# Kernel optimization log

Hardware: AMD Instinct MI355X
Metric: run time of the kernel (lower is better)

The kernel has to match this reference:

```python
import jax, jax.numpy as jnp
import numpy as np

NEG_MASK_SCALE = -1e-09  # faithful to source (source uses -1e-09, likely intended -1e9)


def setup_inputs() -> dict:
    key0 = jax.random.key(0)
    ks = jax.random.split(key0, 7)
    B, Q, K, H = 4, 256, 1024, 128
    return {
        "query": jax.random.normal(ks[0], (B, Q, H), dtype=jnp.float32),
        "key": jax.random.normal(ks[1], (B, K, H), dtype=jnp.float32),
        "value": jax.random.normal(ks[2], (B, K, H), dtype=jnp.float32),
        "mask": jax.random.randint(ks[3], (B, Q, K), 0, 2).astype(jnp.int32),
        "Wq": jax.random.normal(ks[4], (H, H), dtype=jnp.float32) * (1.0 / np.sqrt(H)),
        "Wk": jax.random.normal(ks[5], (H, H), dtype=jnp.float32) * (1.0 / np.sqrt(H)),
        "v": jax.random.normal(ks[6], (H,), dtype=jnp.float32) * (1.0 / np.sqrt(H)),
    }


def reference(query, key, value, mask, Wq, Wk, v):
    # Projections: torch Linear computes x @ W.T
    q_proj = jnp.einsum("bqd,hd->bqh", query, Wq)  # (B, Q, H)
    k_proj = jnp.einsum("bkd,hd->bkh", key, Wk)    # (B, K, H)
    # Additive (Bahdanau) score: v . tanh(q_proj[:, :, None] + k_proj[:, None])
    feat = jnp.tanh(q_proj[:, :, None, :] + k_proj[:, None, :, :])  # (B, Q, K, H)
    score = jnp.einsum("bqkh,h->bqk", feat, v)                      # (B, Q, K)
    score = score + NEG_MASK_SCALE * (1.0 - mask.astype(score.dtype))
    attention_weights = jax.nn.softmax(score, axis=-1)              # (B, Q, K)
    context_vector = jnp.einsum("bqk,bkv->bqv", attention_weights, value)  # (B, Q, V)
    return attention_weights, context_vector
```

## Files before the change

kernel.cpp:

```cpp
#include <hip/hip_runtime.h>

#define Bb 4
#define Qn 256
#define Kn 1024
#define Hn 128
#define QT 4

constexpr float SCALE = 2.88539008177792681f;

#if __has_builtin(__builtin_amdgcn_exp2f)
#define EXP2F(x) __builtin_amdgcn_exp2f(x)
#else
#define EXP2F(x) exp2f(x)
#endif
#if __has_builtin(__builtin_amdgcn_rcpf)
#define RCPF(x) __builtin_amdgcn_rcpf(x)
#else
#define RCPF(x) (1.0f / (x))
#endif

__global__ __launch_bounds__(128) void proj_kernel(const float* __restrict__ query,
                                                   const float* __restrict__ key,
                                                   const float* __restrict__ Wq,
                                                   const float* __restrict__ Wk,
                                                   float* __restrict__ eq,
                                                   float* __restrict__ ekT) {
    __shared__ float4 xs[128];
    const int tid = threadIdx.x;
    const bool isQ = blockIdx.x < (Bb * Qn / 4);
    const int r0 = (isQ ? blockIdx.x : blockIdx.x - Bb * Qn / 4) * 4;
    const float* x = isQ ? query : key;
    const float* W = isQ ? Wq : Wk;

    xs[tid] = ((const float4*)(x + (size_t)r0 * Hn))[tid];
    __syncthreads();
    const float4* W4 = (const float4*)W + (size_t)tid * (Hn / 4);
    float acc0 = 0.f, acc1 = 0.f, acc2 = 0.f, acc3 = 0.f;
#pragma unroll 8
    for (int d = 0; d < Hn / 4; ++d) {
        float4 w = W4[d];
        float4 a0 = xs[d];
        float4 a1 = xs[32 + d];
        float4 a2 = xs[64 + d];
        float4 a3 = xs[96 + d];
        acc0 = fmaf(w.x, a0.x, fmaf(w.y, a0.y, fmaf(w.z, a0.z, fmaf(w.w, a0.w, acc0))));
        acc1 = fmaf(w.x, a1.x, fmaf(w.y, a1.y, fmaf(w.z, a1.z, fmaf(w.w, a1.w, acc1))));
        acc2 = fmaf(w.x, a2.x, fmaf(w.y, a2.y, fmaf(w.z, a2.z, fmaf(w.w, a2.w, acc2))));
        acc3 = fmaf(w.x, a3.x, fmaf(w.y, a3.y, fmaf(w.z, a3.z, fmaf(w.w, a3.w, acc3))));
    }
    if (isQ) {
        eq[(size_t)(r0 + 0) * Hn + tid] = EXP2F(acc0 * SCALE);
        eq[(size_t)(r0 + 1) * Hn + tid] = EXP2F(acc1 * SCALE);
        eq[(size_t)(r0 + 2) * Hn + tid] = EXP2F(acc2 * SCALE);
        eq[(size_t)(r0 + 3) * Hn + tid] = EXP2F(acc3 * SCALE);
    } else {
        const int b = r0 / Kn;
        const int k0 = r0 % Kn;
        float4 res = make_float4(EXP2F(acc0 * SCALE), EXP2F(acc1 * SCALE),
                                 EXP2F(acc2 * SCALE), EXP2F(acc3 * SCALE));
        ((float4*)ekT)[(size_t)(b * Hn + tid) * (Kn / 4) + (k0 >> 2)] = res;
    }
}

__global__ __launch_bounds__(1024) void fused_attn_kernel(const float* __restrict__ eq,
                                                          const float* __restrict__ ekT,
                                                          const float* __restrict__ v,
                                                          const float* __restrict__ value,
                                                          float* __restrict__ attn,
                                                          float* __restrict__ ctx) {
    const int tid = threadIdx.x;
    const int q0 = blockIdx.x * QT;
    const int b = blockIdx.y;

    __shared__ __align__(16) float4 qs4[Hn];
    __shared__ float vs[Hn];
    __shared__ __align__(16) float sc[QT][Kn];
    __shared__ float red[16][QT];
    __shared__ __align__(16) float4 pl[8][QT][Hn / 4];

    if (tid < Hn) vs[tid] = v[tid];
    if (tid < QT * Hn) {
        const int q = tid >> 7, h = tid & 127;
        ((float*)&qs4[h])[q] = eq[((size_t)b * Qn + q0 + q) * Hn + h];
    }
    __syncthreads();

    const int k = tid;
    const float* ek = ekT + (size_t)b * Hn * Kn + k;
    float a0 = 0.f, a1 = 0.f, a2 = 0.f, a3 = 0.f;
#pragma unroll 8
    for (int h = 0; h < Hn; ++h) {
        const float kv = ek[(size_t)h * Kn];
        const float4 qv = qs4[h];
        const float vh = vs[h];
        float r;
        r = RCPF(fmaf(qv.x, kv, 1.0f)); a0 = fmaf(vh, r, a0);
        r = RCPF(fmaf(qv.y, kv, 1.0f)); a1 = fmaf(vh, r, a1);
        r = RCPF(fmaf(qv.z, kv, 1.0f)); a2 = fmaf(vh, r, a2);
        r = RCPF(fmaf(qv.w, kv, 1.0f)); a3 = fmaf(vh, r, a3);
    }

    const int lane = tid & 63, wv = tid >> 6;
    float m0 = a0, m1 = a1, m2 = a2, m3 = a3;
#pragma unroll
    for (int off = 32; off; off >>= 1) {
        m0 = fminf(m0, __shfl_xor(m0, off));
        m1 = fminf(m1, __shfl_xor(m1, off));
        m2 = fminf(m2, __shfl_xor(m2, off));
        m3 = fminf(m3, __shfl_xor(m3, off));
    }
    if (lane == 0) {
        red[wv][0] = m0; red[wv][1] = m1; red[wv][2] = m2; red[wv][3] = m3;
    }
    __syncthreads();
    m0 = red[0][0]; m1 = red[0][1]; m2 = red[0][2]; m3 = red[0][3];
#pragma unroll
    for (int w = 1; w < 16; ++w) {
        m0 = fminf(m0, red[w][0]); m1 = fminf(m1, red[w][1]);
        m2 = fminf(m2, red[w][2]); m3 = fminf(m3, red[w][3]);
    }
    __syncthreads();

    float e0 = EXP2F((m0 - a0) * SCALE);
    float e1 = EXP2F((m1 - a1) * SCALE);
    float e2 = EXP2F((m2 - a2) * SCALE);
    float e3 = EXP2F((m3 - a3) * SCALE);
    float s0 = e0, s1 = e1, s2 = e2, s3 = e3;
#pragma unroll
    for (int off = 32; off; off >>= 1) {
        s0 += __shfl_xor(s0, off);
        s1 += __shfl_xor(s1, off);
        s2 += __shfl_xor(s2, off);
        s3 += __shfl_xor(s3, off);
    }
    if (lane == 0) {
        red[wv][0] = s0; red[wv][1] = s1; red[wv][2] = s2; red[wv][3] = s3;
    }
    __syncthreads();
    s0 = red[0][0]; s1 = red[0][1]; s2 = red[0][2]; s3 = red[0][3];
#pragma unroll
    for (int w = 1; w < 16; ++w) {
        s0 += red[w][0]; s1 += red[w][1]; s2 += red[w][2]; s3 += red[w][3];
    }

    const float w0 = e0 * RCPF(s0);
    const float w1 = e1 * RCPF(s1);
    const float w2 = e2 * RCPF(s2);
    const float w3 = e3 * RCPF(s3);
    sc[0][k] = w0; sc[1][k] = w1; sc[2][k] = w2; sc[3][k] = w3;
    float* arow = attn + ((size_t)b * Qn + q0) * Kn + k;
    arow[0 * Kn] = w0; arow[1 * Kn] = w1; arow[2 * Kn] = w2; arow[3 * Kn] = w3;
    __syncthreads();

    const int kc = tid >> 7;
    const int cq = (tid >> 5) & 3;
    const int h4 = tid & 31;
    const float4* vb = (const float4*)(value + ((size_t)b * Kn + kc * 128) * Hn) + h4;
    const float* wr = &sc[cq][kc * 128];
    float4 acc = make_float4(0.f, 0.f, 0.f, 0.f);
#pragma unroll 4
    for (int kk = 0; kk < 128; ++kk) {
        const float wgt = wr[kk];
        const float4 vv = vb[(size_t)kk * (Hn / 4)];
        acc.x = fmaf(wgt, vv.x, acc.x);
        acc.y = fmaf(wgt, vv.y, acc.y);
        acc.z = fmaf(wgt, vv.z, acc.z);
        acc.w = fmaf(wgt, vv.w, acc.w);
    }
    pl[kc][cq][h4] = acc;
    __syncthreads();
    if (tid < QT * Hn / 4) {
        const int q = tid >> 5, h = tid & 31;
        float4 r0 = pl[0][q][h], r1 = pl[1][q][h], r2 = pl[2][q][h], r3 = pl[3][q][h];
        float4 r4 = pl[4][q][h], r5 = pl[5][q][h], r6 = pl[6][q][h], r7 = pl[7][q][h];
        float4 sum;
        sum.x = ((r0.x + r1.x) + (r2.x + r3.x)) + ((r4.x + r5.x) + (r6.x + r7.x));
        sum.y = ((r0.y + r1.y) + (r2.y + r3.y)) + ((r4.y + r5.y) + (r6.y + r7.y));
        sum.z = ((r0.z + r1.z) + (r2.z + r3.z)) + ((r4.z + r5.z) + (r6.z + r7.z));
        sum.w = ((r0.w + r1.w) + (r2.w + r3.w)) + ((r4.w + r5.w) + (r6.w + r7.w));
        ((float4*)(ctx + ((size_t)b * Qn + q0 + q) * Hn))[h] = sum;
    }
}

extern "C" void kernel_launch(void* const* d_in, const int* in_sizes, int n_in,
                              void* d_out, int out_size, void* d_ws, size_t ws_size,
                              hipStream_t stream) {
    const float* query = (const float*)d_in[0];
    const float* key = (const float*)d_in[1];
    const float* value = (const float*)d_in[2];
    const float* Wq = (const float*)d_in[4];
    const float* Wk = (const float*)d_in[5];
    const float* v = (const float*)d_in[6];

    float* out = (float*)d_out;
    float* attn = out;
    float* ctx = out + (size_t)Bb * Qn * Kn;

    float* ws = (float*)d_ws;
    float* eq = ws;
    float* ekT = ws + 131072;

    proj_kernel<<<dim3(Bb * Qn / 4 + Bb * Kn / 4), dim3(128), 0, stream>>>(
        query, key, Wq, Wk, eq, ekT);
    fused_attn_kernel<<<dim3(Qn / QT, Bb), dim3(1024), 0, stream>>>(
        eq, ekT, v, value, attn, ctx);
}
```

Before: 117.7 us.

## Double-buffer key and value tiles through LDS with register prefetch

The score loop now stages the transposed exp-key matrix through a two-slot shared-memory buffer, eight h-rows at a time. The next chunk is prefetched into registers while the current chunk is computed from LDS. The weighted-value accumulation is restructured the same way, streaming 64-row value chunks through the same buffer, with each k-group handling 8 rows per chunk. This is meant to hide global-memory latency behind the reciprocal/FMA work. In exchange it adds about 64KB of LDS and a block barrier per chunk, roughly 32 extra syncs per block.

```diff
diff --git a/kernel.cpp b/kernel.cpp
--- a/kernel.cpp
+++ b/kernel.cpp
@@ -5,6 +5,10 @@
 #define Kn 1024
 #define Hn 128
 #define QT 4
+#define CH 8
+#define NCH (Hn / CH)
+#define CKV 64
+#define NCKV (Kn / CKV)
 
 constexpr float SCALE = 2.88539008177792681f;
 
@@ -72,6 +76,7 @@
     const int q0 = blockIdx.x * QT;
     const int b = blockIdx.y;
 
+    __shared__ __align__(16) float stage[2][CH * Kn];
     __shared__ __align__(16) float4 qs4[Hn];
     __shared__ float vs[Hn];
     __shared__ __align__(16) float sc[QT][Kn];
@@ -83,21 +88,45 @@
         const int q = tid >> 7, h = tid & 127;
         ((float*)&qs4[h])[q] = eq[((size_t)b * Qn + q0 + q) * Hn + h];
     }
-    __syncthreads();
-
-    const int k = tid;
-    const float* ek = ekT + (size_t)b * Hn * Kn + k;
+
+    const float* ekb = ekT + (size_t)b * Hn * Kn;
+    {
+        const float4* s = (const float4*)ekb;
+        float4 tA = s[tid], tB = s[tid + 1024];
+        ((float4*)&stage[0][0])[tid] = tA;
+        ((float4*)&stage[0][0])[tid + 1024] = tB;
+    }
+    __syncthreads();
+
     float a0 = 0.f, a1 = 0.f, a2 = 0.f, a3 = 0.f;
-#pragma unroll 8
-    for (int h = 0; h < Hn; ++h) {
-        const float kv = ek[(size_t)h * Kn];
-        const float4 qv = qs4[h];
-        const float vh = vs[h];
-        float r;
-        r = RCPF(fmaf(qv.x, kv, 1.0f)); a0 = fmaf(vh, r, a0);
-        r = RCPF(fmaf(qv.y, kv, 1.0f)); a1 = fmaf(vh, r, a1);
-        r = RCPF(fmaf(qv.z, kv, 1.0f)); a2 = fmaf(vh, r, a2);
-        r = RCPF(fmaf(qv.w, kv, 1.0f)); a3 = fmaf(vh, r, a3);
+    for (int c = 0; c < NCH; ++c) {
+        const int cur = c & 1;
+        const bool more = (c + 1 < NCH);
+        float4 tA, tB;
+        if (more) {
+            const float4* s = (const float4*)(ekb + (size_t)(c + 1) * CH * Kn);
+            tA = s[tid];
+            tB = s[tid + 1024];
+        }
+        const float* sb = &stage[cur][0];
+#pragma unroll
+        for (int j = 0; j < CH; ++j) {
+            const int h = c * CH + j;
+            const float kv = sb[j * Kn + tid];
+            const float4 qv = qs4[h];
+            const float vh = vs[h];
+            float r;
+            r = RCPF(fmaf(qv.x, kv, 1.0f)); a0 = fmaf(vh, r, a0);
+            r = RCPF(fmaf(qv.y, kv, 1.0f)); a1 = fmaf(vh, r, a1);
+            r = RCPF(fmaf(qv.z, kv, 1.0f)); a2 = fmaf(vh, r, a2);
+            r = RCPF(fmaf(qv.w, kv, 1.0f)); a3 = fmaf(vh, r, a3);
+        }
+        if (more) {
+            float* db = &stage[cur ^ 1][0];
+            ((float4*)db)[tid] = tA;
+            ((float4*)db)[tid + 1024] = tB;
+        }
+        __syncthreads();
     }
 
     const int lane = tid & 63, wv = tid >> 6;
@@ -143,6 +172,7 @@
         s0 += red[w][0]; s1 += red[w][1]; s2 += red[w][2]; s3 += red[w][3];
     }
 
+    const int k = tid;
     const float w0 = e0 * RCPF(s0);
     const float w1 = e1 * RCPF(s1);
     const float w2 = e2 * RCPF(s2);
@@ -150,24 +180,49 @@
     sc[0][k] = w0; sc[1][k] = w1; sc[2][k] = w2; sc[3][k] = w3;
     float* arow = attn + ((size_t)b * Qn + q0) * Kn + k;
     arow[0 * Kn] = w0; arow[1 * Kn] = w1; arow[2 * Kn] = w2; arow[3 * Kn] = w3;
-    __syncthreads();
-
-    const int kc = tid >> 7;
+
+    const float* vbase = value + (size_t)b * Kn * Hn;
+    {
+        const float4* s = (const float4*)vbase;
+        float4 tA = s[tid], tB = s[tid + 1024];
+        __syncthreads();
+        ((float4*)&stage[0][0])[tid] = tA;
+        ((float4*)&stage[0][0])[tid + 1024] = tB;
+    }
+    __syncthreads();
+
+    const int kc2 = tid >> 7;
     const int cq = (tid >> 5) & 3;
     const int h4 = tid & 31;
-    const float4* vb = (const float4*)(value + ((size_t)b * Kn + kc * 128) * Hn) + h4;
-    const float* wr = &sc[cq][kc * 128];
     float4 acc = make_float4(0.f, 0.f, 0.f, 0.f);
-#pragma unroll 4
-    for (int kk = 0; kk < 128; ++kk) {
-        const float wgt = wr[kk];
-        const float4 vv = vb[(size_t)kk * (Hn / 4)];
-        acc.x = fmaf(wgt, vv.x, acc.x);
-        acc.y = fmaf(wgt, vv.y, acc.y);
-        acc.z = fmaf(wgt, vv.z, acc.z);
-        acc.w = fmaf(wgt, vv.w, acc.w);
-    }
-    pl[kc][cq][h4] = acc;
+    for (int c = 0; c < NCKV; ++c) {
+        const int cur = c & 1;
+        const bool more = (c + 1 < NCKV);
+        float4 tA, tB;
+        if (more) {
+            const float4* s = (const float4*)(vbase + (size_t)(c + 1) * CKV * Hn);
+            tA = s[tid];
+            tB = s[tid + 1024];
+        }
+        const float* wr = &sc[cq][c * CKV + kc2 * 8];
+        const float4* vl = (const float4*)&stage[cur][(size_t)kc2 * 8 * Hn] + h4;
+#pragma unroll
+        for (int j = 0; j < 8; ++j) {
+            const float wgt = wr[j];
+            const float4 vv = vl[(size_t)j * (Hn / 4)];
+            acc.x = fmaf(wgt, vv.x, acc.x);
+            acc.y = fmaf(wgt, vv.y, acc.y);
+            acc.z = fmaf(wgt, vv.z, acc.z);
+            acc.w = fmaf(wgt, vv.w, acc.w);
+        }
+        if (more) {
+            float* db = &stage[cur ^ 1][0];
+            ((float4*)db)[tid] = tA;
+            ((float4*)db)[tid + 1024] = tB;
+        }
+        __syncthreads();
+    }
+    pl[kc2][cq][h4] = acc;
     __syncthreads();
     if (tid < QT * Hn / 4) {
         const int q = tid >> 5, h = tid & 31;
```

After: 119.0 us. No clear change (+1.1%).
